# Performance work log

Measured on AMD Instinct MI355X. Metric: run time of the kernel, lower is better.

Reference implementation:

```python
import jax, jax.numpy as jnp
import numpy as np

D = 128
NQ = 25  # r2d2 quantized AP: 25 triangular bins over similarity range [0, 1]


def grid_sample_bilinear(img, grid):
    """F.grid_sample, mode='bilinear', padding_mode='zeros', align_corners=False.
    img: (B,C,H,W), grid: (B,Hg,Wg,2) in [-1,1] (x, y order). -> (B,C,Hg,Wg)"""
    B, C, H, W = img.shape
    gx = ((grid[..., 0] + 1.0) * W - 1.0) * 0.5  # (B,Hg,Wg) unnormalized x
    gy = ((grid[..., 1] + 1.0) * H - 1.0) * 0.5
    x0f = jnp.floor(gx)
    y0f = jnp.floor(gy)
    wx1 = gx - x0f
    wy1 = gy - y0f
    x0 = x0f.astype(jnp.int32)
    y0 = y0f.astype(jnp.int32)

    def gather(yi, xi):
        valid = ((xi >= 0) & (xi < W) & (yi >= 0) & (yi < H)).astype(img.dtype)
        xc = jnp.clip(xi, 0, W - 1)
        yc = jnp.clip(yi, 0, H - 1)
        v = jax.vmap(lambda im, y, x: im[:, y, x])(img, yc, xc)  # (B,C,Hg,Wg)
        return v * valid[:, None]

    out = (gather(y0, x0) * ((1 - wy1) * (1 - wx1))[:, None]
           + gather(y0, x0 + 1) * ((1 - wy1) * wx1)[:, None]
           + gather(y0 + 1, x0) * (wy1 * (1 - wx1))[:, None]
           + gather(y0 + 1, x0 + 1) * (wy1 * wx1)[:, None])
    return out


def quantized_ap(sim, lab):
    """r2d2 QAPLoss: soft-histogram differentiable AP.
    sim: (B,N,M) similarities, lab: (B,N,M) binary labels (float). -> (B,N) AP per query."""
    a = jnp.float32(NQ - 1)                 # slope; bin width = 1/a over gap [0,1]
    c = jnp.linspace(1.0, 0.0, NQ, dtype=sim.dtype)  # bin centers, descending score
    # triangular kernel membership: relu(1 - a*|s - c|), shape (B,N,Q,M)
    q = jnp.maximum(0.0, 1.0 - a * jnp.abs(sim[:, :, None, :] - c[None, None, :, None]))
    nbs = q.sum(-1)                          # (B,N,Q) soft count per bin
    rec = (q * lab[:, :, None, :]).sum(-1)   # (B,N,Q) soft positive count per bin
    prec = jnp.cumsum(rec, -1) / (1e-16 + jnp.cumsum(nbs, -1))
    rec = rec / rec.sum(-1, keepdims=True)
    return (prec * rec).sum(-1)              # (B,N)


def setup_inputs() -> dict:
    key = jax.random.key(0)
    k1, k2, k3, k4, k5 = jax.random.split(key, 5)
    B, H, W = 2, 32, 32
    d1 = jax.random.normal(k1, (B, D, H, W), dtype=jnp.float32)
    d2 = jax.random.normal(k2, (B, D, H, W), dtype=jnp.float32)
    # L2-normalize over channels (r2d2 descriptors are unit-norm -> sims in [-1,1])
    d1 = d1 / jnp.linalg.norm(d1, axis=1, keepdims=True)
    d2 = d2 / jnp.linalg.norm(d2, axis=1, keepdims=True)
    rel = jax.random.uniform(k3, (B, 1, H, W), dtype=jnp.float32)
    grid = jax.random.uniform(k4, (B, H, W, 2), dtype=jnp.float32) * 1.8 - 0.9  # in [-0.9,0.9]
    label = jax.random.randint(k5, (B, H, W, H, W), 0, 2, dtype=jnp.int32)
    return {"desc1": d1, "desc2": d2, "reliability": rel, "grid": grid, "label": label}


def reference(desc1, desc2, reliability, grid, label):
    B, C, H, W = desc1.shape
    d2w = grid_sample_bilinear(desc2, grid)           # warp image2 descriptors
    q = desc1.reshape(B, C, H * W).transpose(0, 2, 1)  # (B,N,C)
    db = d2w.reshape(B, C, H * W).transpose(0, 2, 1)   # (B,M,C)
    sim = jnp.einsum('bnd,bmd->bnm', q, db)            # per-sample pairwise similarity
    lab = label.reshape(B, H * W, H * W).astype(sim.dtype)
    ap = quantized_ap(sim, lab)                        # (B,N)
    return jnp.mean(ap)                                # mAP over queries and batch
```

## Files before the change

kernel.cpp:

```cpp
#include <hip/hip_runtime.h>


#define NQB 25

template<int CTRL>
__device__ __forceinline__ float dppadd(float v) {
    int s = __builtin_amdgcn_update_dpp(0, __float_as_int(v), CTRL, 0xf, 0xf, true);
    return v + __int_as_float(s);
}
__device__ __forceinline__ float red16(float v) {
    v = dppadd<0xB1>(v);
    v = dppadd<0x4E>(v);
    v = dppadd<0x141>(v);
    v = dppadd<0x140>(v);
    return v;
}

__device__ __forceinline__ void loadc(const float* __restrict__ dp, int ch,
                                      float* d)
{
    int cb = ch << 3;
#pragma unroll
    for (int i = 0; i < 8; i++) {
        d[i]     = dp[(size_t)(cb + i) << 10];
        d[8 + i] = dp[(((size_t)(cb + i)) << 10) + 512];
    }
}
__device__ __forceinline__ void fmac(const float* __restrict__ d1, int ch,
                                     const float* d, float* a0, float* a1)
{
    int cb = ch << 3;
#pragma unroll
    for (int i = 0; i < 8; i++) {
        const float* qp = d1 + ((size_t)(cb + i) << 10);
#pragma unroll
        for (int qq = 0; qq < 8; qq++) {
            float qv = qp[qq];
            a0[qq] = fmaf(qv, d[i], a0[qq]);
            a1[qq] = fmaf(qv, d[8 + i], a1[qq]);
        }
    }
}

__global__ __launch_bounds__(512) void k_main(const float* __restrict__ desc1,
                                              const float* __restrict__ desc2,
                                              const float* __restrict__ grd,
                                              const int* __restrict__ label,
                                              float* __restrict__ appart)
{
    __shared__ float s[8][1024];
    __shared__ float CNs[8][4][NQB];
    __shared__ float CRs[8][4][NQB];
    __shared__ float apb[8];

    int tid = threadIdx.x;
    int qg0 = blockIdx.x << 3;
    int b = qg0 >> 10;
    int n0 = qg0 & 1023;

    int q = tid >> 6, l = tid & 63;
    const int* lp = label + ((size_t)(qg0 + q) << 10) + l;
    int lv[16];
#pragma unroll
    for (int e = 0; e < 16; e++) lv[e] = lp[(size_t)(e << 6)];
    const float2* gp = (const float2*)grd + ((size_t)b << 10) + l;
    float2 gv[16];
#pragma unroll
    for (int e = 0; e < 16; e++) gv[e] = gp[(size_t)(e << 6)];

    const float* d1 = desc1 + ((size_t)b << 17) + n0;
    const float* dp = desc2 + ((size_t)b << 17) + tid;

    float a0[8], a1[8];
#pragma unroll
    for (int qq = 0; qq < 8; qq++) { a0[qq] = 0.f; a1[qq] = 0.f; }

    float dA[16], dB[16];
    loadc(dp, 0, dA);
    for (int ch = 0; ch < 16; ch += 2) {
        loadc(dp, ch + 1, dB);
        fmac(d1, ch, dA, a0, a1);
        if (ch + 2 < 16) loadc(dp, ch + 2, dA);
        fmac(d1, ch + 1, dB, a0, a1);
    }
#pragma unroll
    for (int qq = 0; qq < 8; qq++) { s[qq][tid] = a0[qq]; s[qq][tid + 512] = a1[qq]; }
    __syncthreads();

    float CN[NQB], CR[NQB];
#pragma unroll
    for (int k = 0; k < NQB; k++) { CN[k] = 0.f; CR[k] = 0.f; }
    const float* sq = s[q];
#pragma unroll
    for (int e = 0; e < 16; e++) {
        float gx = gv[e].x, gy = gv[e].y;
        float fx = ((gx + 1.f) * 32.f - 1.f) * 0.5f;
        float fy = ((gy + 1.f) * 32.f - 1.f) * 0.5f;
        float x0f = floorf(fx), y0f = floorf(fy);
        float wx1 = fx - x0f, wy1 = fy - y0f;
        float wx0 = 1.f - wx1, wy0 = 1.f - wy1;
        int x0 = (int)x0f, y0 = (int)y0f;
        float w00 = wy0 * wx0;
        float w01 = wy0 * wx1;
        float w10 = wy1 * wx0;
        float w11 = wy1 * wx1;
        int base = (y0 << 5) + x0;
        float2 v0 = *(const float2*)&sq[base];
        float2 v1 = *(const float2*)&sq[base + 32];
        float sv = w00 * v0.x;
        sv = fmaf(w01, v0.y, sv);
        sv = fmaf(w10, v1.x, sv);
        sv = fmaf(w11, v1.y, sv);

        float u = fmaf(-24.f, sv, 24.f);
        float lfv = (float)lv[e];
#pragma unroll
        for (int k = 0; k < NQB; k++) {
            float t = fminf(fmaxf((float)(k + 1) - u, 0.f), 1.f);
            CN[k] += t;
            CR[k] = fmaf(lfv, t, CR[k]);
        }
    }
#pragma unroll
    for (int k = 0; k < NQB; k++) { CN[k] = red16(CN[k]); CR[k] = red16(CR[k]); }
    if ((l & 15) == 0) {
        int rec = l >> 4;
#pragma unroll
        for (int k = 0; k < NQB; k++) { CNs[q][rec][k] = CN[k]; CRs[q][rec][k] = CR[k]; }
    }
    __syncthreads();

    if (tid < 8) {
        float ap = 0.f, prev = 0.f;
#pragma unroll
        for (int k = 0; k < NQB; k++) {
            float cn = CNs[tid][0][k] + CNs[tid][1][k] + CNs[tid][2][k] + CNs[tid][3][k];
            float cr = CRs[tid][0][k] + CRs[tid][1][k] + CRs[tid][2][k] + CRs[tid][3][k];
            float pr = cr / (1e-16f + cn);
            ap += pr * (cr - prev);
            prev = cr;
        }
        apb[tid] = ap / prev;
    }
    __syncthreads();
    if (tid == 0) {
        float v = 0.f;
#pragma unroll
        for (int q2 = 0; q2 < 8; q2++) v += apb[q2];
        appart[blockIdx.x] = v;
    }
}

__global__ __launch_bounds__(256) void k_final(const float* __restrict__ appart,
                                               float* __restrict__ out,
                                               int nb, float invn)
{
    int tid = threadIdx.x;
    float v = 0.f;
    for (int i = tid; i < nb; i += 256) v += appart[i];
    for (int off = 32; off; off >>= 1) v += __shfl_xor(v, off, 64);
    __shared__ float wsum[4];
    if ((tid & 63) == 0) wsum[tid >> 6] = v;
    __syncthreads();
    if (tid == 0) out[0] = (wsum[0] + wsum[1] + wsum[2] + wsum[3]) * invn;
}

extern "C" void kernel_launch(void* const* d_in, const int* in_sizes, int n_in,
                              void* d_out, int out_size, void* d_ws, size_t ws_size,
                              hipStream_t stream)
{
    const float* desc1 = (const float*)d_in[0];
    const float* desc2 = (const float*)d_in[1];
    const float* grd   = (const float*)d_in[3];
    const int*   label = (const int*)d_in[4];

    int B = in_sizes[0] / (128 * 1024);
    int npos = B * 1024;
    int nblk = npos / 8;

    float* ws = (float*)d_ws;
    float* appart = ws;
    float* out = (float*)d_out;

    k_main<<<nblk, 512, 0, stream>>>(desc1, desc2, grd, label, appart);
    k_final<<<1, 256, 0, stream>>>(appart, out, nblk, 1.f / (float)npos);
}
```

Baseline: 28.01 us.

## Compute similarity with bf16x3 split MFMA after a descriptor prep kernel

Adds a prep kernel that splits desc1 and desc2 into three bf16 parts each, stored transposed or in fragment layout in the workspace. The main kernel then computes the per-query similarity row with 16x16x32 bf16 MFMAs, keeping six cross terms to approximate fp32 accuracy, in place of scalar FP32 FMAs. This is meant to offload the dot-product work to the matrix cores. In exchange it adds an extra launch and a round trip of the split data through global memory, and half of each A tile is wasted on zero padding because only 8 queries fill the 16 rows.

```diff
diff --git a/kernel.cpp b/kernel.cpp
--- a/kernel.cpp
+++ b/kernel.cpp
@@ -1,7 +1,12 @@
 #include <hip/hip_runtime.h>
+#include <hip/hip_bf16.h>
 
 
 #define NQB 25
+
+typedef __attribute__((ext_vector_type(8))) short    bf16x8;
+typedef __attribute__((ext_vector_type(8))) unsigned short us8;
+typedef __attribute__((ext_vector_type(4))) float    f32x4;
 
 template<int CTRL>
 __device__ __forceinline__ float dppadd(float v) {
@@ -16,37 +21,87 @@
     return v;
 }
 
-__device__ __forceinline__ void loadc(const float* __restrict__ dp, int ch,
-                                      float* d)
-{
-    int cb = ch << 3;
-#pragma unroll
-    for (int i = 0; i < 8; i++) {
-        d[i]     = dp[(size_t)(cb + i) << 10];
-        d[8 + i] = dp[(((size_t)(cb + i)) << 10) + 512];
-    }
-}
-__device__ __forceinline__ void fmac(const float* __restrict__ d1, int ch,
-                                     const float* d, float* a0, float* a1)
-{
-    int cb = ch << 3;
-#pragma unroll
-    for (int i = 0; i < 8; i++) {
-        const float* qp = d1 + ((size_t)(cb + i) << 10);
-#pragma unroll
-        for (int qq = 0; qq < 8; qq++) {
-            float qv = qp[qq];
-            a0[qq] = fmaf(qv, d[i], a0[qq]);
-            a1[qq] = fmaf(qv, d[8 + i], a1[qq]);
-        }
-    }
-}
-
-__global__ __launch_bounds__(512) void k_main(const float* __restrict__ desc1,
+__device__ __forceinline__ void split3(float x, unsigned short& o1,
+                                       unsigned short& o2, unsigned short& o3)
+{
+    __hip_bfloat16 b1 = __float2bfloat16(x);
+    float r = x - __bfloat162float(b1);
+    __hip_bfloat16 b2 = __float2bfloat16(r);
+    r = r - __bfloat162float(b2);
+    __hip_bfloat16 b3 = __float2bfloat16(r);
+    o1 = __builtin_bit_cast(unsigned short, b1);
+    o2 = __builtin_bit_cast(unsigned short, b2);
+    o3 = __builtin_bit_cast(unsigned short, b3);
+}
+
+__global__ __launch_bounds__(256) void k_prep(const float* __restrict__ desc1,
                                               const float* __restrict__ desc2,
+                                              unsigned short* __restrict__ d1s,
+                                              unsigned short* __restrict__ d2f,
+                                              int npos)
+{
+    __shared__ float t32[32][33];
+    __shared__ float tile[128][17];
+    int B = npos >> 10;
+    int bid = blockIdx.x, tid = threadIdx.x;
+    size_t sstride = (size_t)npos * 128;
+
+    if (bid < B * 32) {
+        int b = bid >> 5, n0 = (bid & 31) << 5;
+        for (int c0 = 0; c0 < 128; c0 += 32) {
+            int i = tid >> 5, j = tid & 31;
+#pragma unroll
+            for (int r = 0; r < 4; ++r) {
+                int cl = i + (r << 3);
+                t32[cl][j] = desc1[((size_t)(b * 128 + c0 + cl) << 10) + n0 + j];
+            }
+            __syncthreads();
+            int nl = tid >> 3, cg = tid & 7;
+#pragma unroll
+            for (int cc = 0; cc < 4; ++cc) {
+                int cl = (cg << 2) + cc;
+                unsigned short s1, s2, s3;
+                split3(t32[cl][nl], s1, s2, s3);
+                size_t idx = ((size_t)(b << 10) + n0 + nl) * 128 + c0 + cl;
+                d1s[idx] = s1;
+                d1s[sstride + idx] = s2;
+                d1s[2 * sstride + idx] = s3;
+            }
+            __syncthreads();
+        }
+    } else {
+        int r2 = bid - B * 32;
+        int b = r2 >> 6, pt = r2 & 63;
+        int p0 = pt << 4;
+#pragma unroll
+        for (int it = 0; it < 8; ++it) {
+            int c = (tid >> 4) + (it << 4);
+            int pp = tid & 15;
+            tile[c][pp] = desc2[((size_t)(b * 128 + c) << 10) + p0 + pp];
+        }
+        __syncthreads();
+        int l = tid & 63, kt = tid >> 6;
+        us8 o1, o2, o3;
+#pragma unroll
+        for (int j = 0; j < 8; ++j) {
+            int c = (kt << 5) + ((l >> 4) << 3) + j;
+            unsigned short s1, s2, s3;
+            split3(tile[c][l & 15], s1, s2, s3);
+            o1[j] = s1; o2[j] = s2; o3[j] = s3;
+        }
+        size_t bi = (((size_t)(b * 64 + pt) * 4 + kt) << 6) + l;
+        us8* dst = (us8*)d2f;
+        size_t s8 = sstride >> 3;
+        dst[bi] = o1; dst[s8 + bi] = o2; dst[2 * s8 + bi] = o3;
+    }
+}
+
+__global__ __launch_bounds__(512) void k_main(const unsigned short* __restrict__ d1s,
+                                              const unsigned short* __restrict__ d2f,
                                               const float* __restrict__ grd,
                                               const int* __restrict__ label,
-                                              float* __restrict__ appart)
+                                              float* __restrict__ appart,
+                                              int npos)
 {
     __shared__ float s[8][1024];
     __shared__ float CNs[8][4][NQB];
@@ -56,7 +111,6 @@
     int tid = threadIdx.x;
     int qg0 = blockIdx.x << 3;
     int b = qg0 >> 10;
-    int n0 = qg0 & 1023;
 
     int q = tid >> 6, l = tid & 63;
     const int* lp = label + ((size_t)(qg0 + q) << 10) + l;
@@ -68,23 +122,50 @@
 #pragma unroll
     for (int e = 0; e < 16; e++) gv[e] = gp[(size_t)(e << 6)];
 
-    const float* d1 = desc1 + ((size_t)b << 17) + n0;
-    const float* dp = desc2 + ((size_t)b << 17) + tid;
-
-    float a0[8], a1[8];
-#pragma unroll
-    for (int qq = 0; qq < 8; qq++) { a0[qq] = 0.f; a1[qq] = 0.f; }
-
-    float dA[16], dB[16];
-    loadc(dp, 0, dA);
-    for (int ch = 0; ch < 16; ch += 2) {
-        loadc(dp, ch + 1, dB);
-        fmac(d1, ch, dA, a0, a1);
-        if (ch + 2 < 16) loadc(dp, ch + 2, dA);
-        fmac(d1, ch + 1, dB, a0, a1);
-    }
-#pragma unroll
-    for (int qq = 0; qq < 8; qq++) { s[qq][tid] = a0[qq]; s[qq][tid + 512] = a1[qq]; }
+    int w = q;
+    int col = l & 15, kg = l >> 4;
+    size_t s8 = (size_t)npos * 16;
+    const bf16x8* A8 = (const bf16x8*)d1s;
+    const bf16x8* B8 = (const bf16x8*)d2f;
+
+    f32x4 acc[8];
+#pragma unroll
+    for (int nt = 0; nt < 8; ++nt) acc[nt] = (f32x4){0.f, 0.f, 0.f, 0.f};
+
+    bool aval = col < 8;
+    size_t abase = ((size_t)(qg0 + (col & 7)) << 4) + kg;
+    size_t bbase = (((size_t)(b << 6) + (w << 3)) << 8) + l;
+    bf16x8 zf = {0, 0, 0, 0, 0, 0, 0, 0};
+
+#pragma unroll
+    for (int kt = 0; kt < 4; ++kt) {
+        bf16x8 A0 = aval ? A8[abase + (kt << 2)] : zf;
+        bf16x8 A1 = aval ? A8[s8 + abase + (kt << 2)] : zf;
+        bf16x8 A2 = aval ? A8[2 * s8 + abase + (kt << 2)] : zf;
+#pragma unroll
+        for (int nt = 0; nt < 8; ++nt) {
+            size_t bi = bbase + ((size_t)nt << 8) + (kt << 6);
+            bf16x8 B0 = B8[bi];
+            bf16x8 B1 = B8[s8 + bi];
+            bf16x8 B2 = B8[2 * s8 + bi];
+            f32x4 a = acc[nt];
+            a = __builtin_amdgcn_mfma_f32_16x16x32_bf16(A0, B0, a, 0, 0, 0);
+            a = __builtin_amdgcn_mfma_f32_16x16x32_bf16(A0, B1, a, 0, 0, 0);
+            a = __builtin_amdgcn_mfma_f32_16x16x32_bf16(A1, B0, a, 0, 0, 0);
+            a = __builtin_amdgcn_mfma_f32_16x16x32_bf16(A0, B2, a, 0, 0, 0);
+            a = __builtin_amdgcn_mfma_f32_16x16x32_bf16(A2, B0, a, 0, 0, 0);
+            a = __builtin_amdgcn_mfma_f32_16x16x32_bf16(A1, B1, a, 0, 0, 0);
+            acc[nt] = a;
+        }
+    }
+    if (l < 32) {
+        int qh = l >> 4;
+#pragma unroll
+        for (int nt = 0; nt < 8; ++nt)
+#pragma unroll
+            for (int r = 0; r < 4; ++r)
+                s[(qh << 2) + r][(w << 7) + (nt << 4) + col] = acc[nt][r];
+    }
     __syncthreads();
 
     float CN[NQB], CR[NQB];
@@ -178,10 +259,14 @@
     int npos = B * 1024;
     int nblk = npos / 8;
 
-    float* ws = (float*)d_ws;
-    float* appart = ws;
+    char* ws = (char*)d_ws;
+    float* appart = (float*)ws;
+    size_t off = ((size_t)nblk * 4 + 15) & ~(size_t)15;
+    unsigned short* d1s = (unsigned short*)(ws + off);
+    unsigned short* d2f = d1s + (size_t)3 * npos * 128;
     float* out = (float*)d_out;
 
-    k_main<<<nblk, 512, 0, stream>>>(desc1, desc2, grd, label, appart);
+    k_prep<<<B * 96, 256, 0, stream>>>(desc1, desc2, d1s, d2f, npos);
+    k_main<<<nblk, 512, 0, stream>>>(d1s, d2f, grd, label, appart, npos);
     k_final<<<1, 256, 0, stream>>>(appart, out, nblk, 1.f / (float)npos);
 }
```

Result: slower. 38.75 us (+38.3%).
